# Optimization experiments

Hardware: AMD Instinct MI355X
Metric: run time of the kernel (lower is better)

The kernel has to match this reference:

```python
import jax, jax.numpy as jnp
import numpy as np
from jax import lax

B, S, D, L, HID = 256, 512, 64, 64, 256  # batch, seq_len, input_dim, latent_dim, MLP hidden


def setup_inputs() -> dict:
    key = jax.random.key(0)
    ks = jax.random.split(key, 16)
    sc = 0.05  # small init scale for MLP weights

    def eye_noise(k, n):
        # identity init (as in nn.Parameter(torch.eye)) plus small noise so inverse is non-trivial
        return jnp.eye(n, dtype=jnp.float32) + 0.05 * jax.random.normal(k, (n, n), dtype=jnp.float32)

    return {
        "x": jax.random.normal(ks[0], (B, S, D), dtype=jnp.float32),
        "eps": jax.random.normal(ks[1], (B, S, L), dtype=jnp.float32),
        "enc_w1": sc * jax.random.normal(ks[2], (D, HID), dtype=jnp.float32),
        "enc_b1": jnp.zeros((HID,), dtype=jnp.float32),
        "enc_w2": sc * jax.random.normal(ks[3], (HID, 2 * L), dtype=jnp.float32),
        "enc_b2": jnp.zeros((2 * L,), dtype=jnp.float32),
        "dec_w1": sc * jax.random.normal(ks[4], (L, HID), dtype=jnp.float32),
        "dec_b1": jnp.zeros((HID,), dtype=jnp.float32),
        "dec_w2": sc * jax.random.normal(ks[5], (HID, D), dtype=jnp.float32),
        "dec_b2": jnp.zeros((D,), dtype=jnp.float32),
        "A": eye_noise(ks[6], L),   # transition_matrix
        "Q": eye_noise(ks[7], L),   # process_covariance
        "Hm": eye_noise(ks[8], L),  # measurement_matrix
        "R": eye_noise(ks[9], L),   # measurement_covariance
    }


def reference(x, eps, enc_w1, enc_b1, enc_w2, enc_b2,
              dec_w1, dec_b1, dec_w2, dec_b2, A, Q, Hm, R):
    Bb, Ss, _ = x.shape
    # ---- encoder on all timesteps at once (no temporal dependency) ----
    h = jax.nn.relu(jnp.einsum('bsd,dh->bsh', x, enc_w1) + enc_b1)
    ml = jnp.einsum('bsh,hk->bsk', h, enc_w2) + enc_b2          # [B,S,2L]
    z_mean, z_logvar = jnp.split(ml, 2, axis=-1)                 # [B,S,L] each
    z = z_mean + eps * jnp.exp(0.5 * z_logvar)                   # reparameterize

    # ---- Kalman recursion; covariances don't depend on state in source, hoist ----
    AQ = A @ Q                                                   # z_pred_cov
    innov_cov = Hm @ AQ + R
    K = AQ @ jnp.linalg.inv(innov_cov)                           # kalman gain [L,L]

    def step(z_prev, inputs):
        x_t, z_t = inputs                                        # [B,D], [B,L]
        z_pred = z_prev @ A.T + z_t                              # (A @ z_prev^T)^T + z
        innovation = x_t - z_pred @ Hm.T
        z_up = z_pred + innovation @ K.T
        return z_up, z_up

    xs = (jnp.swapaxes(x, 0, 1), jnp.swapaxes(z, 0, 1))          # time-major [S,B,*]
    z0 = jnp.zeros((Bb, L), dtype=x.dtype)
    _, z_upd = lax.scan(step, z0, xs)                            # [S,B,L]
    z_upd = jnp.swapaxes(z_upd, 0, 1)                            # [B,S,L]

    # ---- decoder ----
    hd = jax.nn.relu(jnp.einsum('bsl,lh->bsh', z_upd, dec_w1) + dec_b1)
    x_recon = jax.nn.sigmoid(jnp.einsum('bsh,hd->bsd', hd, dec_w2) + dec_b2)

    return x_recon, z_mean.reshape(-1, L), z_logvar.reshape(-1, L)
```

## Files before the change

### kernel.cpp

```cpp
#include <hip/hip_runtime.h>
#include <hip/hip_bf16.h>


typedef short short8 __attribute__((ext_vector_type(8)));
typedef float f32x4 __attribute__((ext_vector_type(4)));

#define OUTSEG 8388608

__device__ __forceinline__ unsigned short f2bf(float f) {
    unsigned int u = __builtin_bit_cast(unsigned int, f);
    u += 0x7fffu + ((u >> 16) & 1u);
    return (unsigned short)(u >> 16);
}
__device__ __forceinline__ float bf2f(unsigned short h) {
    unsigned int u = ((unsigned int)h) << 16;
    return __builtin_bit_cast(float, u);
}
__device__ __forceinline__ float rlf(float v, int l) {
    return __builtin_bit_cast(float, __builtin_amdgcn_readlane(__builtin_bit_cast(int, v), l));
}
__device__ __forceinline__ float matvec_rl(const float* m, float z, float c) {
    float a0 = c, a1 = 0.f, a2 = 0.f, a3 = 0.f;
#pragma unroll
    for (int k = 0; k < 64; k += 4) {
        a0 = fmaf(m[k + 0], rlf(z, k + 0), a0);
        a1 = fmaf(m[k + 1], rlf(z, k + 1), a1);
        a2 = fmaf(m[k + 2], rlf(z, k + 2), a2);
        a3 = fmaf(m[k + 3], rlf(z, k + 3), a3);
    }
    return (a0 + a1) + (a2 + a3);
}
__device__ __forceinline__ void load_mrow(const float* Mp, int j, float* m) {
#pragma unroll
    for (int q = 0; q < 16; q++) {
        float4 v = *reinterpret_cast<const float4*>(&Mp[j * 64 + q * 4]);
        m[q * 4 + 0] = v.x; m[q * 4 + 1] = v.y;
        m[q * 4 + 2] = v.z; m[q * 4 + 3] = v.w;
    }
}

__device__ void mm64(const float* A, int lda, const float* B, int ldb,
                     float* C, int ldc, int mode, const float* Add, int ldadd,
                     int tid) {
    int i = tid & 63;
    int j0 = (tid >> 6) * 16;
    float acc[16];
#pragma unroll
    for (int jj = 0; jj < 16; jj++) acc[jj] = 0.f;
    for (int k = 0; k < 64; k++) {
        float a = A[i * lda + k];
#pragma unroll
        for (int jj = 0; jj < 16; jj++) acc[jj] += a * B[k * ldb + j0 + jj];
    }
#pragma unroll
    for (int jj = 0; jj < 16; jj++) {
        int j = j0 + jj;
        float v = acc[jj];
        if (mode == 1) v += Add[i * ldadd + j];
        if (mode == 2) v = ((i == j) ? 1.f : 0.f) - v;
        C[i * ldc + j] = v;
    }
}

__device__ void load64(const float* g, float* L, int tid) {
    for (int idx = tid; idx < 4096; idx += 256)
        L[(idx >> 6) * 65 + (idx & 63)] = g[idx];
}

__device__ void tr_tile(const float* src, int sld, unsigned short* dst, int dld,
                        int r0, int c0, int tid, float* LT) {
    int rr = tid >> 2, q = tid & 3;
#pragma unroll
    for (int u = 0; u < 4; u++) {
        float4 v = *reinterpret_cast<const float4*>(
            &src[(size_t)(r0 + rr) * sld + c0 + q * 16 + u * 4]);
        LT[rr * 65 + q * 16 + u * 4 + 0] = v.x;
        LT[rr * 65 + q * 16 + u * 4 + 1] = v.y;
        LT[rr * 65 + q * 16 + u * 4 + 2] = v.z;
        LT[rr * 65 + q * 16 + u * 4 + 3] = v.w;
    }
    __syncthreads();
    short8 s0, s1;
#pragma unroll
    for (int u = 0; u < 8; u++) s0[u] = (short)f2bf(LT[(q * 16 + u) * 65 + rr]);
#pragma unroll
    for (int u = 0; u < 8; u++) s1[u] = (short)f2bf(LT[(q * 16 + 8 + u) * 65 + rr]);
    *reinterpret_cast<short8*>(&dst[(size_t)(c0 + rr) * dld + r0 + q * 16]) = s0;
    *reinterpret_cast<short8*>(&dst[(size_t)(c0 + rr) * dld + r0 + q * 16 + 8]) = s1;
}

__global__ __launch_bounds__(256) void kprep(
    const float* __restrict__ Ain, const float* __restrict__ Qin,
    const float* __restrict__ Hin, const float* __restrict__ Rin,
    const float* __restrict__ ew1, const float* __restrict__ ew2,
    const float* __restrict__ dw1, const float* __restrict__ dw2,
    float* __restrict__ Mw, float* __restrict__ M16w,
    unsigned short* __restrict__ Gb, unsigned short* __restrict__ Kb,
    unsigned short* __restrict__ w1t, unsigned short* __restrict__ w2t,
    unsigned short* __restrict__ d1t, unsigned short* __restrict__ d2t) {
    __shared__ float La[64 * 65], Lb[64 * 65], Lc[64 * 65];
    __shared__ float aug[64 * 129];
    __shared__ int s_piv;
    __shared__ float s_pv;
    int tid = threadIdx.x;

    if (blockIdx.x != 0) {
        int t = blockIdx.x - 1;
        const float* src; unsigned short* dst; int sld, dld, r0, c0;
        if (t < 4)       { src = ew1; dst = w1t; sld = 256; dld = 64;  r0 = 0;             c0 = t * 64; }
        else if (t < 12) { int i = t - 4;  src = ew2; dst = w2t; sld = 128; dld = 256; r0 = (i >> 1) * 64; c0 = (i & 1) * 64; }
        else if (t < 16) { int i = t - 12; src = dw1; dst = d1t; sld = 256; dld = 64;  r0 = 0;             c0 = i * 64; }
        else             { int i = t - 16; src = dw2; dst = d2t; sld = 64;  dld = 256; r0 = i * 64;        c0 = 0; }
        tr_tile(src, sld, dst, dld, r0, c0, tid, La);
        return;
    }

    load64(Ain, La, tid);
    load64(Qin, Lb, tid);
    __syncthreads();
    mm64(La, 65, Lb, 65, Lc, 65, 0, nullptr, 0, tid);
    __syncthreads();
    load64(Hin, La, tid);
    load64(Rin, Lb, tid);
    __syncthreads();
    mm64(La, 65, Lc, 65, aug, 129, 1, Lb, 65, tid);
    for (int idx = tid; idx < 4096; idx += 256) {
        int i = idx >> 6, j = idx & 63;
        aug[i * 129 + 64 + j] = (i == j) ? 1.f : 0.f;
    }
    __syncthreads();

    for (int k = 0; k < 64; k++) {
        if (tid < 64) {
            float v = (tid >= k) ? fabsf(aug[tid * 129 + k]) : -1.f;
            int ix = tid;
#pragma unroll
            for (int off = 1; off < 64; off <<= 1) {
                float ov = __shfl_xor(v, off);
                int oi = __shfl_xor(ix, off);
                if (ov > v) { v = ov; ix = oi; }
            }
            if (tid == 0) { s_piv = ix; s_pv = aug[ix * 129 + k]; }
        }
        __syncthreads();
        int p = s_piv;
        float rp = 1.0f / s_pv;
        if (p != k) {
            for (int idx = tid; idx < 129; idx += 256) {
                float t1 = aug[k * 129 + idx];
                aug[k * 129 + idx] = aug[p * 129 + idx];
                aug[p * 129 + idx] = t1;
            }
            __syncthreads();
        }
        int i = tid & 63, jb = tid >> 6;
        float mlt = aug[i * 129 + k] * rp;
        float pv[33], rw[33];
#pragma unroll
        for (int jj = 0; jj < 33; jj++) {
            int j = jb + 4 * jj;
            if (j < 129) { pv[jj] = aug[k * 129 + j]; rw[jj] = aug[i * 129 + j]; }
        }
        __syncthreads();
#pragma unroll
        for (int jj = 0; jj < 33; jj++) {
            int j = jb + 4 * jj;
            if (j < 129) aug[i * 129 + j] = (i == k) ? pv[jj] * rp : rw[jj] - mlt * pv[jj];
        }
        __syncthreads();
    }

    mm64(Lc, 65, aug + 64, 129, Lb, 65, 0, nullptr, 0, tid);
    __syncthreads();
    mm64(Lb, 65, La, 65, Lc, 65, 2, nullptr, 0, tid);
    __syncthreads();
    for (int idx = tid; idx < 4096; idx += 256) {
        int i = idx >> 6, j = idx & 63;
        Kb[idx] = f2bf(Lb[i * 65 + j]);
        Gb[idx] = f2bf(Lc[i * 65 + j]);
    }
    load64(Ain, La, tid);
    __syncthreads();
    mm64(Lc, 65, La, 65, aug, 129, 0, nullptr, 0, tid);
    __syncthreads();
    for (int idx = tid; idx < 4096; idx += 256)
        Mw[idx] = aug[(idx >> 6) * 129 + (idx & 63)];
    __syncthreads();
    mm64(aug, 129, aug, 129, Lb, 65, 0, nullptr, 0, tid);
    __syncthreads();
    mm64(Lb, 65, Lb, 65, Lc, 65, 0, nullptr, 0, tid);
    __syncthreads();
    mm64(Lc, 65, Lc, 65, La, 65, 0, nullptr, 0, tid);
    __syncthreads();
    mm64(La, 65, La, 65, Lb, 65, 0, nullptr, 0, tid);
    __syncthreads();
    for (int idx = tid; idx < 4096; idx += 256)
        M16w[idx] = Lb[(idx >> 6) * 65 + (idx & 63)];
}

__global__ __launch_bounds__(256) void kenc(
    const float* __restrict__ x, const float* __restrict__ eps,
    const float* __restrict__ b1, const float* __restrict__ b2,
    const unsigned short* __restrict__ w1t, const unsigned short* __restrict__ w2t,
    const unsigned short* __restrict__ Gb, const unsigned short* __restrict__ Kb,
    const float* __restrict__ Mw, unsigned short* __restrict__ cbuf,
    float* __restrict__ Pbuf, float* __restrict__ zmean,
    float* __restrict__ zlogv) {
    __shared__ unsigned short Xs[64][72];
    __shared__ unsigned short Hs[64][264];
    __shared__ unsigned short Zs[64][72];
    int row0 = blockIdx.x * 64;
    int tid = threadIdx.x;
    int lane = tid & 63, w = tid >> 6;
    int ml = lane & 15, kg = lane >> 4;

    {
        int r = tid >> 2, c0 = (tid & 3) * 16;
        const float4* xp = reinterpret_cast<const float4*>(&x[(size_t)(row0 + r) * 64 + c0]);
        float4 v0 = xp[0], v1 = xp[1], v2 = xp[2], v3 = xp[3];
        short8 s0, s1;
        s0[0] = (short)f2bf(v0.x); s0[1] = (short)f2bf(v0.y);
        s0[2] = (short)f2bf(v0.z); s0[3] = (short)f2bf(v0.w);
        s0[4] = (short)f2bf(v1.x); s0[5] = (short)f2bf(v1.y);
        s0[6] = (short)f2bf(v1.z); s0[7] = (short)f2bf(v1.w);
        s1[0] = (short)f2bf(v2.x); s1[1] = (short)f2bf(v2.y);
        s1[2] = (short)f2bf(v2.z); s1[3] = (short)f2bf(v2.w);
        s1[4] = (short)f2bf(v3.x); s1[5] = (short)f2bf(v3.y);
        s1[6] = (short)f2bf(v3.z); s1[7] = (short)f2bf(v3.w);
        *reinterpret_cast<short8*>(&Xs[r][c0]) = s0;
        *reinterpret_cast<short8*>(&Xs[r][c0 + 8]) = s1;
    }
    __syncthreads();

    short8 afr[4][2];
#pragma unroll
    for (int mt = 0; mt < 4; mt++)
#pragma unroll
        for (int kb = 0; kb < 2; kb++)
            afr[mt][kb] = *reinterpret_cast<const short8*>(&Xs[mt * 16 + ml][kb * 32 + kg * 8]);

#pragma unroll
    for (int q = 0; q < 4; q++) {
        int nt = w * 4 + q;
        f32x4 acc[4];
#pragma unroll
        for (int mt = 0; mt < 4; mt++) acc[mt] = (f32x4){0.f, 0.f, 0.f, 0.f};
#pragma unroll
        for (int kb = 0; kb < 2; kb++) {
            short8 bfr = *reinterpret_cast<const short8*>(&w1t[(nt * 16 + ml) * 64 + kb * 32 + kg * 8]);
#pragma unroll
            for (int mt = 0; mt < 4; mt++)
                acc[mt] = __builtin_amdgcn_mfma_f32_16x16x32_bf16(afr[mt][kb], bfr, acc[mt], 0, 0, 0);
        }
        float bias = b1[nt * 16 + ml];
#pragma unroll
        for (int mt = 0; mt < 4; mt++)
#pragma unroll
            for (int i = 0; i < 4; i++) {
                float v = acc[mt][i] + bias;
                v = v > 0.f ? v : 0.f;
                Hs[mt * 16 + kg * 4 + i][nt * 16 + ml] = f2bf(v);
            }
    }
    __syncthreads();

    f32x4 acc2[2][4];
#pragma unroll
    for (int p = 0; p < 2; p++)
#pragma unroll
        for (int mt = 0; mt < 4; mt++) acc2[p][mt] = (f32x4){0.f, 0.f, 0.f, 0.f};
#pragma unroll
    for (int kb = 0; kb < 8; kb++) {
        short8 a2[4];
#pragma unroll
        for (int mt = 0; mt < 4; mt++)
            a2[mt] = *reinterpret_cast<const short8*>(&Hs[mt * 16 + ml][kb * 32 + kg * 8]);
#pragma unroll
        for (int p = 0; p < 2; p++) {
            int nt = w + 4 * p;
            short8 bfr = *reinterpret_cast<const short8*>(&w2t[(nt * 16 + ml) * 256 + kb * 32 + kg * 8]);
#pragma unroll
            for (int mt = 0; mt < 4; mt++)
                acc2[p][mt] = __builtin_amdgcn_mfma_f32_16x16x32_bf16(a2[mt], bfr, acc2[p][mt], 0, 0, 0);
        }
    }
    int colz = w * 16 + ml;
    float bm = b2[colz], bl = b2[64 + colz];
#pragma unroll
    for (int mt = 0; mt < 4; mt++)
#pragma unroll
        for (int i = 0; i < 4; i++) {
            int r = mt * 16 + kg * 4 + i;
            size_t grow = (size_t)(row0 + r);
            float zm = acc2[0][mt][i] + bm;
            float zl = acc2[1][mt][i] + bl;
            zmean[grow * 64 + colz] = zm;
            zlogv[grow * 64 + colz] = zl;
            float zz = zm + eps[grow * 64 + colz] * expf(0.5f * zl);
            Zs[r][colz] = f2bf(zz);
        }
    __syncthreads();

    f32x4 acc3[4];
#pragma unroll
    for (int mt = 0; mt < 4; mt++) acc3[mt] = (f32x4){0.f, 0.f, 0.f, 0.f};
    short8 az[4][2];
#pragma unroll
    for (int mt = 0; mt < 4; mt++)
#pragma unroll
        for (int kb = 0; kb < 2; kb++)
            az[mt][kb] = *reinterpret_cast<const short8*>(&Zs[mt * 16 + ml][kb * 32 + kg * 8]);
#pragma unroll
    for (int kb = 0; kb < 2; kb++) {
        short8 bg = *reinterpret_cast<const short8*>(&Gb[(w * 16 + ml) * 64 + kb * 32 + kg * 8]);
        short8 bk = *reinterpret_cast<const short8*>(&Kb[(w * 16 + ml) * 64 + kb * 32 + kg * 8]);
#pragma unroll
        for (int mt = 0; mt < 4; mt++)
            acc3[mt] = __builtin_amdgcn_mfma_f32_16x16x32_bf16(az[mt][kb], bg, acc3[mt], 0, 0, 0);
#pragma unroll
        for (int mt = 0; mt < 4; mt++)
            acc3[mt] = __builtin_amdgcn_mfma_f32_16x16x32_bf16(afr[mt][kb], bk, acc3[mt], 0, 0, 0);
    }
#pragma unroll
    for (int mt = 0; mt < 4; mt++)
#pragma unroll
        for (int i = 0; i < 4; i++)
            Xs[mt * 16 + kg * 4 + i][colz] = f2bf(acc3[mt][i]);
    __syncthreads();

    {
        int r = tid >> 2, c0 = (tid & 3) * 16;
        short8 s0 = *reinterpret_cast<const short8*>(&Xs[r][c0]);
        short8 s1 = *reinterpret_cast<const short8*>(&Xs[r][c0 + 8]);
        *reinterpret_cast<short8*>(&cbuf[(size_t)(row0 + r) * 64 + c0]) = s0;
        *reinterpret_cast<short8*>(&cbuf[(size_t)(row0 + r) * 64 + c0 + 8]) = s1;
    }

    {
        int j = lane;
        float m[64];
        load_mrow(Mw, j, m);
        unsigned short cv[16];
#pragma unroll
        for (int t = 0; t < 16; t++) cv[t] = Xs[w * 16 + t][j];
        float z = bf2f(cv[0]);
#pragma unroll
        for (int t = 1; t < 16; t++) z = matvec_rl(m, z, bf2f(cv[t]));
        int b = row0 >> 9;
        int chunk = ((row0 & 511) >> 4) + w;
        if (chunk != 31)
            Pbuf[((size_t)b * 32 + chunk + 1) * 64 + j] = z;
    }
}

__global__ __launch_bounds__(64) void kchain(const float* __restrict__ M16w,
                                             float* __restrict__ Pbuf) {
    int b = blockIdx.x, j = threadIdx.x;
    float m[64];
    load_mrow(M16w, j, m);
    float* P = Pbuf + (size_t)b * 32 * 64;
    P[j] = 0.f;
    float z = 0.f;
    for (int c = 1; c < 32; c++) {
        float f = P[c * 64 + j];
        z = matvec_rl(m, z, f);
        P[c * 64 + j] = z;
    }
}

__global__ __launch_bounds__(256) void kdec(float* __restrict__ xr,
                                            const float* __restrict__ db1,
                                            const float* __restrict__ db2,
                                            const unsigned short* __restrict__ d1t,
                                            const unsigned short* __restrict__ d2t,
                                            const float* __restrict__ Mw,
                                            const float* __restrict__ Pbuf,
                                            const unsigned short* __restrict__ cbuf) {
    __shared__ unsigned short Zs[64][72];
    __shared__ unsigned short Hs[64][264];
    int row0 = blockIdx.x * 64;
    int tid = threadIdx.x;
    int lane = tid & 63, w = tid >> 6;
    int ml = lane & 15, kg = lane >> 4;

    {
        int j = lane;
        int b = row0 >> 9;
        int chunk = ((row0 & 511) >> 4) + w;
        float m[64];
        load_mrow(Mw, j, m);
        float z = Pbuf[((size_t)b * 32 + chunk) * 64 + j];
        const unsigned short* cb = cbuf + ((size_t)row0 + w * 16) * 64;
        unsigned short cv[16];
#pragma unroll
        for (int t = 0; t < 16; t++) cv[t] = cb[t * 64 + j];
#pragma unroll
        for (int t = 0; t < 16; t++) {
            z = matvec_rl(m, z, bf2f(cv[t]));
            Zs[w * 16 + t][j] = f2bf(z);
        }
    }
    __syncthreads();

    short8 afr[4][2];
#pragma unroll
    for (int mt = 0; mt < 4; mt++)
#pragma unroll
        for (int kb = 0; kb < 2; kb++)
            afr[mt][kb] = *reinterpret_cast<const short8*>(&Zs[mt * 16 + ml][kb * 32 + kg * 8]);

#pragma unroll
    for (int q = 0; q < 4; q++) {
        int nt = w * 4 + q;
        f32x4 acc[4];
#pragma unroll
        for (int mt = 0; mt < 4; mt++) acc[mt] = (f32x4){0.f, 0.f, 0.f, 0.f};
#pragma unroll
        for (int kb = 0; kb < 2; kb++) {
            short8 bfr = *reinterpret_cast<const short8*>(&d1t[(nt * 16 + ml) * 64 + kb * 32 + kg * 8]);
#pragma unroll
            for (int mt = 0; mt < 4; mt++)
                acc[mt] = __builtin_amdgcn_mfma_f32_16x16x32_bf16(afr[mt][kb], bfr, acc[mt], 0, 0, 0);
        }
        float bias = db1[nt * 16 + ml];
#pragma unroll
        for (int mt = 0; mt < 4; mt++)
#pragma unroll
            for (int i = 0; i < 4; i++) {
                float v = acc[mt][i] + bias;
                v = v > 0.f ? v : 0.f;
                Hs[mt * 16 + kg * 4 + i][nt * 16 + ml] = f2bf(v);
            }
    }
    __syncthreads();

    f32x4 acc2[4];
#pragma unroll
    for (int mt = 0; mt < 4; mt++) acc2[mt] = (f32x4){0.f, 0.f, 0.f, 0.f};
#pragma unroll
    for (int kb = 0; kb < 8; kb++) {
        short8 bfr = *reinterpret_cast<const short8*>(&d2t[(w * 16 + ml) * 256 + kb * 32 + kg * 8]);
#pragma unroll
        for (int mt = 0; mt < 4; mt++) {
            short8 a2 = *reinterpret_cast<const short8*>(&Hs[mt * 16 + ml][kb * 32 + kg * 8]);
            acc2[mt] = __builtin_amdgcn_mfma_f32_16x16x32_bf16(a2, bfr, acc2[mt], 0, 0, 0);
        }
    }
    float bias2 = db2[w * 16 + ml];
#pragma unroll
    for (int mt = 0; mt < 4; mt++)
#pragma unroll
        for (int i = 0; i < 4; i++) {
            int r = mt * 16 + kg * 4 + i;
            float v = acc2[mt][i] + bias2;
            float s = 1.f / (1.f + expf(-v));
            xr[(size_t)(row0 + r) * 64 + w * 16 + ml] = s;
        }
}

extern "C" void kernel_launch(void* const* d_in, const int* in_sizes, int n_in,
                              void* d_out, int out_size, void* d_ws, size_t ws_size,
                              hipStream_t stream) {
    (void)in_sizes; (void)n_in; (void)out_size; (void)ws_size;
    const float* x      = (const float*)d_in[0];
    const float* eps    = (const float*)d_in[1];
    const float* enc_w1 = (const float*)d_in[2];
    const float* enc_b1 = (const float*)d_in[3];
    const float* enc_w2 = (const float*)d_in[4];
    const float* enc_b2 = (const float*)d_in[5];
    const float* dec_w1 = (const float*)d_in[6];
    const float* dec_b1 = (const float*)d_in[7];
    const float* dec_w2 = (const float*)d_in[8];
    const float* dec_b2 = (const float*)d_in[9];
    const float* Ain    = (const float*)d_in[10];
    const float* Qin    = (const float*)d_in[11];
    const float* Hin    = (const float*)d_in[12];
    const float* Rin    = (const float*)d_in[13];

    float* out   = (float*)d_out;
    float* xrec  = out;
    float* zmean = out + OUTSEG;
    float* zlogv = out + 2 * OUTSEG;

    char* ws = (char*)d_ws;
    float*          Mw   = (float*)(ws);
    float*          M16w = (float*)(ws + 16384);
    unsigned short* Gb   = (unsigned short*)(ws + 32768);
    unsigned short* Kb   = (unsigned short*)(ws + 40960);
    unsigned short* w1t  = (unsigned short*)(ws + 49152);
    unsigned short* w2t  = (unsigned short*)(ws + 81920);
    unsigned short* d1t  = (unsigned short*)(ws + 147456);
    unsigned short* d2t  = (unsigned short*)(ws + 180224);
    float*          Pbuf = (float*)(ws + 212992);
    unsigned short* cbuf = (unsigned short*)(ws + 2310144);

    hipLaunchKernelGGL(kprep, dim3(21), dim3(256), 0, stream,
                       Ain, Qin, Hin, Rin, enc_w1, enc_w2, dec_w1, dec_w2,
                       Mw, M16w, Gb, Kb, w1t, w2t, d1t, d2t);
    hipLaunchKernelGGL(kenc, dim3(2048), dim3(256), 0, stream,
                       x, eps, enc_b1, enc_b2, w1t, w2t, Gb, Kb, Mw, cbuf, Pbuf,
                       zmean, zlogv);
    hipLaunchKernelGGL(kchain, dim3(256), dim3(64), 0, stream, M16w, Pbuf);
    hipLaunchKernelGGL(kdec, dim3(2048), dim3(256), 0, stream,
                       xrec, dec_b1, dec_b2, d1t, d2t, Mw, Pbuf, cbuf);
}
```

Baseline: 424.2 us.

## Overlap Kalman matrix prep with encoder by splitting encoder into two kernels

The serial single-block Kalman precompute (gain, inverse, matrix powers) moves out of its own prep kernel into block 0 of a new encoder kernel, so it runs concurrently with the encoder MLP blocks. The encoder is split in two: kenc1 computes the MLP and stages bf16 z in the x_recon output buffer, and kenc2 applies G and K and does the intra-chunk recurrence. The Gauss-Jordan inverse is rewritten to keep rows in registers without pivoting, and kchain prefetches the next chunk value. The cost is an extra launch plus a global round trip for z, and dropping pivoting adds numerical risk.

```diff
diff --git a/kernel.cpp b/kernel.cpp
--- a/kernel.cpp
+++ b/kernel.cpp
@@ -37,34 +37,6 @@
         m[q * 4 + 0] = v.x; m[q * 4 + 1] = v.y;
         m[q * 4 + 2] = v.z; m[q * 4 + 3] = v.w;
     }
-}
-
-__device__ void mm64(const float* A, int lda, const float* B, int ldb,
-                     float* C, int ldc, int mode, const float* Add, int ldadd,
-                     int tid) {
-    int i = tid & 63;
-    int j0 = (tid >> 6) * 16;
-    float acc[16];
-#pragma unroll
-    for (int jj = 0; jj < 16; jj++) acc[jj] = 0.f;
-    for (int k = 0; k < 64; k++) {
-        float a = A[i * lda + k];
-#pragma unroll
-        for (int jj = 0; jj < 16; jj++) acc[jj] += a * B[k * ldb + j0 + jj];
-    }
-#pragma unroll
-    for (int jj = 0; jj < 16; jj++) {
-        int j = j0 + jj;
-        float v = acc[jj];
-        if (mode == 1) v += Add[i * ldadd + j];
-        if (mode == 2) v = ((i == j) ? 1.f : 0.f) - v;
-        C[i * ldc + j] = v;
-    }
-}
-
-__device__ void load64(const float* g, float* L, int tid) {
-    for (int idx = tid; idx < 4096; idx += 256)
-        L[(idx >> 6) * 65 + (idx & 63)] = g[idx];
 }
 
 __device__ void tr_tile(const float* src, int sld, unsigned short* dst, int dld,
@@ -89,128 +61,181 @@
     *reinterpret_cast<short8*>(&dst[(size_t)(c0 + rr) * dld + r0 + q * 16 + 8]) = s1;
 }
 
-__global__ __launch_bounds__(256) void kprep(
-    const float* __restrict__ Ain, const float* __restrict__ Qin,
-    const float* __restrict__ Hin, const float* __restrict__ Rin,
+__global__ __launch_bounds__(256) void ktr(
     const float* __restrict__ ew1, const float* __restrict__ ew2,
     const float* __restrict__ dw1, const float* __restrict__ dw2,
-    float* __restrict__ Mw, float* __restrict__ M16w,
-    unsigned short* __restrict__ Gb, unsigned short* __restrict__ Kb,
     unsigned short* __restrict__ w1t, unsigned short* __restrict__ w2t,
     unsigned short* __restrict__ d1t, unsigned short* __restrict__ d2t) {
-    __shared__ float La[64 * 65], Lb[64 * 65], Lc[64 * 65];
-    __shared__ float aug[64 * 129];
-    __shared__ int s_piv;
-    __shared__ float s_pv;
+    __shared__ float La[64 * 65];
     int tid = threadIdx.x;
-
-    if (blockIdx.x != 0) {
-        int t = blockIdx.x - 1;
-        const float* src; unsigned short* dst; int sld, dld, r0, c0;
-        if (t < 4)       { src = ew1; dst = w1t; sld = 256; dld = 64;  r0 = 0;             c0 = t * 64; }
-        else if (t < 12) { int i = t - 4;  src = ew2; dst = w2t; sld = 128; dld = 256; r0 = (i >> 1) * 64; c0 = (i & 1) * 64; }
-        else if (t < 16) { int i = t - 12; src = dw1; dst = d1t; sld = 256; dld = 64;  r0 = 0;             c0 = i * 64; }
-        else             { int i = t - 16; src = dw2; dst = d2t; sld = 64;  dld = 256; r0 = i * 64;        c0 = 0; }
-        tr_tile(src, sld, dst, dld, r0, c0, tid, La);
-        return;
-    }
-
-    load64(Ain, La, tid);
-    load64(Qin, Lb, tid);
-    __syncthreads();
-    mm64(La, 65, Lb, 65, Lc, 65, 0, nullptr, 0, tid);
-    __syncthreads();
-    load64(Hin, La, tid);
-    load64(Rin, Lb, tid);
-    __syncthreads();
-    mm64(La, 65, Lc, 65, aug, 129, 1, Lb, 65, tid);
+    int t = blockIdx.x;
+    const float* src; unsigned short* dst; int sld, dld, r0, c0;
+    if (t < 4)       { src = ew1; dst = w1t; sld = 256; dld = 64;  r0 = 0;             c0 = t * 64; }
+    else if (t < 12) { int i = t - 4;  src = ew2; dst = w2t; sld = 128; dld = 256; r0 = (i >> 1) * 64; c0 = (i & 1) * 64; }
+    else if (t < 16) { int i = t - 12; src = dw1; dst = d1t; sld = 256; dld = 64;  r0 = 0;             c0 = i * 64; }
+    else             { int i = t - 16; src = dw2; dst = d2t; sld = 64;  dld = 256; r0 = i * 64;        c0 = 0; }
+    tr_tile(src, sld, dst, dld, r0, c0, tid, La);
+}
+
+__device__ __noinline__ void mmc(const float* Ag, const float* Bg, float* Cg,
+                                 float* Lx, int mode, const float* Dg,
+                                 unsigned short* Cb, int tid) {
+    for (int idx = tid; idx < 4096; idx += 256)
+        Lx[(idx >> 6) * 68 + (idx & 63)] = Bg[idx];
+    __syncthreads();
+    int i = tid & 63, j0 = (tid >> 6) * 16;
+    float4 a4[16];
+#pragma unroll
+    for (int q = 0; q < 16; q++)
+        a4[q] = reinterpret_cast<const float4*>(Ag + i * 64)[q];
+    float acc[16];
+#pragma unroll
+    for (int jj = 0; jj < 16; jj++) acc[jj] = 0.f;
+#pragma unroll
+    for (int q = 0; q < 16; q++) {
+        float av[4] = {a4[q].x, a4[q].y, a4[q].z, a4[q].w};
+#pragma unroll
+        for (int t = 0; t < 4; t++) {
+            int k = q * 4 + t;
+            const float4* Br = reinterpret_cast<const float4*>(&Lx[k * 68 + j0]);
+            float4 b0 = Br[0], b1 = Br[1], b2 = Br[2], b3 = Br[3];
+            acc[0]  = fmaf(av[t], b0.x, acc[0]);
+            acc[1]  = fmaf(av[t], b0.y, acc[1]);
+            acc[2]  = fmaf(av[t], b0.z, acc[2]);
+            acc[3]  = fmaf(av[t], b0.w, acc[3]);
+            acc[4]  = fmaf(av[t], b1.x, acc[4]);
+            acc[5]  = fmaf(av[t], b1.y, acc[5]);
+            acc[6]  = fmaf(av[t], b1.z, acc[6]);
+            acc[7]  = fmaf(av[t], b1.w, acc[7]);
+            acc[8]  = fmaf(av[t], b2.x, acc[8]);
+            acc[9]  = fmaf(av[t], b2.y, acc[9]);
+            acc[10] = fmaf(av[t], b2.z, acc[10]);
+            acc[11] = fmaf(av[t], b2.w, acc[11]);
+            acc[12] = fmaf(av[t], b3.x, acc[12]);
+            acc[13] = fmaf(av[t], b3.y, acc[13]);
+            acc[14] = fmaf(av[t], b3.z, acc[14]);
+            acc[15] = fmaf(av[t], b3.w, acc[15]);
+        }
+    }
+#pragma unroll
+    for (int jj = 0; jj < 16; jj++) {
+        int j = j0 + jj;
+        float v = acc[jj];
+        if (mode == 1) v += Dg[i * 64 + j];
+        if (mode == 2) v = ((i == j) ? 1.f : 0.f) - v;
+        Cg[i * 64 + j] = v;
+        if (Cb) Cb[i * 64 + j] = f2bf(v);
+    }
+    __syncthreads();
+}
+
+__device__ void chain_block(char* smem, const float* Ain, const float* Qin,
+                            const float* Hin, const float* Rin,
+                            float* AQg, float* Sg, float* Kg, float* Gg,
+                            float* T1, float* T2, float* Mw, float* M16w,
+                            unsigned short* Gb, unsigned short* Kb) {
+    float* aug = (float*)smem;
+    float* Lx  = (float*)(smem + 33024);
+    float* prow2 = Lx;
+    float* mcol  = Lx + 128;
+    int tid = threadIdx.x;
+
+    mmc(Ain, Qin, AQg, Lx, 0, nullptr, nullptr, tid);
+    mmc(Hin, AQg, Sg, Lx, 1, Rin, nullptr, tid);
+
+    for (int idx = tid; idx < 8192; idx += 256) {
+        int i = idx & 63, j = idx >> 6;
+        float v = (j < 64) ? Sg[j * 64 + i] : AQg[(j - 64) * 64 + i];
+        aug[i * 129 + j] = v;
+    }
+    __syncthreads();
+
+    int i = tid & 63, jb = tid >> 6;
+    float r[32];
+#pragma unroll
+    for (int u = 0; u < 32; u++) r[u] = aug[i * 129 + jb + 4 * u];
+    __syncthreads();
+
+    for (int k = 0; k < 64; k++) {
+        if (i == k) {
+#pragma unroll
+            for (int q = 0; q < 8; q++) {
+                float4 v4 = {r[4 * q], r[4 * q + 1], r[4 * q + 2], r[4 * q + 3]};
+                *reinterpret_cast<float4*>(&prow2[jb * 32 + 4 * q]) = v4;
+            }
+        }
+        if (jb == (k & 3)) {
+            int usel = k >> 2;
+            float v = r[0];
+#pragma unroll
+            for (int u = 1; u < 32; u++) v = (u == usel) ? r[u] : v;
+            mcol[i] = v;
+        }
+        __syncthreads();
+        float pv = prow2[(k & 3) * 32 + (k >> 2)];
+        float rp = 1.0f / pv;
+        float m = (i == k) ? (1.0f - rp) : mcol[i] * rp;
+#pragma unroll
+        for (int q = 0; q < 8; q++) {
+            float4 p4 = *reinterpret_cast<const float4*>(&prow2[jb * 32 + 4 * q]);
+            r[4 * q + 0] = fmaf(-m, p4.x, r[4 * q + 0]);
+            r[4 * q + 1] = fmaf(-m, p4.y, r[4 * q + 1]);
+            r[4 * q + 2] = fmaf(-m, p4.z, r[4 * q + 2]);
+            r[4 * q + 3] = fmaf(-m, p4.w, r[4 * q + 3]);
+        }
+        __syncthreads();
+    }
+
+    float* Ktmp = aug;
+#pragma unroll
+    for (int u = 16; u < 32; u++) {
+        int jc = jb + 4 * (u - 16);
+        Ktmp[jc * 64 + i] = r[u];
+    }
+    __syncthreads();
     for (int idx = tid; idx < 4096; idx += 256) {
-        int i = idx >> 6, j = idx & 63;
-        aug[i * 129 + 64 + j] = (i == j) ? 1.f : 0.f;
-    }
-    __syncthreads();
-
-    for (int k = 0; k < 64; k++) {
-        if (tid < 64) {
-            float v = (tid >= k) ? fabsf(aug[tid * 129 + k]) : -1.f;
-            int ix = tid;
-#pragma unroll
-            for (int off = 1; off < 64; off <<= 1) {
-                float ov = __shfl_xor(v, off);
-                int oi = __shfl_xor(ix, off);
-                if (ov > v) { v = ov; ix = oi; }
-            }
-            if (tid == 0) { s_piv = ix; s_pv = aug[ix * 129 + k]; }
-        }
-        __syncthreads();
-        int p = s_piv;
-        float rp = 1.0f / s_pv;
-        if (p != k) {
-            for (int idx = tid; idx < 129; idx += 256) {
-                float t1 = aug[k * 129 + idx];
-                aug[k * 129 + idx] = aug[p * 129 + idx];
-                aug[p * 129 + idx] = t1;
-            }
-            __syncthreads();
-        }
-        int i = tid & 63, jb = tid >> 6;
-        float mlt = aug[i * 129 + k] * rp;
-        float pv[33], rw[33];
-#pragma unroll
-        for (int jj = 0; jj < 33; jj++) {
-            int j = jb + 4 * jj;
-            if (j < 129) { pv[jj] = aug[k * 129 + j]; rw[jj] = aug[i * 129 + j]; }
-        }
-        __syncthreads();
-#pragma unroll
-        for (int jj = 0; jj < 33; jj++) {
-            int j = jb + 4 * jj;
-            if (j < 129) aug[i * 129 + j] = (i == k) ? pv[jj] * rp : rw[jj] - mlt * pv[jj];
-        }
-        __syncthreads();
-    }
-
-    mm64(Lc, 65, aug + 64, 129, Lb, 65, 0, nullptr, 0, tid);
-    __syncthreads();
-    mm64(Lb, 65, La, 65, Lc, 65, 2, nullptr, 0, tid);
-    __syncthreads();
-    for (int idx = tid; idx < 4096; idx += 256) {
-        int i = idx >> 6, j = idx & 63;
-        Kb[idx] = f2bf(Lb[i * 65 + j]);
-        Gb[idx] = f2bf(Lc[i * 65 + j]);
-    }
-    load64(Ain, La, tid);
-    __syncthreads();
-    mm64(Lc, 65, La, 65, aug, 129, 0, nullptr, 0, tid);
-    __syncthreads();
-    for (int idx = tid; idx < 4096; idx += 256)
-        Mw[idx] = aug[(idx >> 6) * 129 + (idx & 63)];
-    __syncthreads();
-    mm64(aug, 129, aug, 129, Lb, 65, 0, nullptr, 0, tid);
-    __syncthreads();
-    mm64(Lb, 65, Lb, 65, Lc, 65, 0, nullptr, 0, tid);
-    __syncthreads();
-    mm64(Lc, 65, Lc, 65, La, 65, 0, nullptr, 0, tid);
-    __syncthreads();
-    mm64(La, 65, La, 65, Lb, 65, 0, nullptr, 0, tid);
-    __syncthreads();
-    for (int idx = tid; idx < 4096; idx += 256)
-        M16w[idx] = Lb[(idx >> 6) * 65 + (idx & 63)];
-}
-
-__global__ __launch_bounds__(256) void kenc(
+        float v = Ktmp[idx];
+        Kg[idx] = v;
+        Kb[idx] = f2bf(v);
+    }
+    __syncthreads();
+
+    mmc(Kg, Hin, Gg, Lx, 2, nullptr, Gb, tid);
+    mmc(Gg, Ain, Mw, Lx, 0, nullptr, nullptr, tid);
+    mmc(Mw, Mw, T1, Lx, 0, nullptr, nullptr, tid);
+    mmc(T1, T1, T2, Lx, 0, nullptr, nullptr, tid);
+    mmc(T2, T2, T1, Lx, 0, nullptr, nullptr, tid);
+    mmc(T1, T1, M16w, Lx, 0, nullptr, nullptr, tid);
+}
+
+__global__ __launch_bounds__(256) void kenc1(
     const float* __restrict__ x, const float* __restrict__ eps,
     const float* __restrict__ b1, const float* __restrict__ b2,
     const unsigned short* __restrict__ w1t, const unsigned short* __restrict__ w2t,
-    const unsigned short* __restrict__ Gb, const unsigned short* __restrict__ Kb,
-    const float* __restrict__ Mw, unsigned short* __restrict__ cbuf,
-    float* __restrict__ Pbuf, float* __restrict__ zmean,
-    float* __restrict__ zlogv) {
-    __shared__ unsigned short Xs[64][72];
-    __shared__ unsigned short Hs[64][264];
-    __shared__ unsigned short Zs[64][72];
-    int row0 = blockIdx.x * 64;
+    unsigned short* __restrict__ zstg, float* __restrict__ zmean,
+    float* __restrict__ zlogv,
+    const float* __restrict__ Ain, const float* __restrict__ Qin,
+    const float* __restrict__ Hin, const float* __restrict__ Rin,
+    float* __restrict__ AQg, float* __restrict__ Sg, float* __restrict__ Kg,
+    float* __restrict__ Gg, float* __restrict__ T1, float* __restrict__ T2,
+    float* __restrict__ Mw, float* __restrict__ M16w,
+    unsigned short* __restrict__ Gb, unsigned short* __restrict__ Kb) {
+    __shared__ __align__(16) char smem[52224];
     int tid = threadIdx.x;
+
+    if (blockIdx.x == 0) {
+        chain_block(smem, Ain, Qin, Hin, Rin, AQg, Sg, Kg, Gg, T1, T2,
+                    Mw, M16w, Gb, Kb);
+        return;
+    }
+
+    typedef unsigned short (*T72)[72];
+    typedef unsigned short (*T264)[264];
+    T72  Xs = (T72)(smem);
+    T264 Hs = (T264)(smem + 9216);
+    T72  Zs = (T72)(smem + 43008);
+
+    int row0 = (blockIdx.x - 1) * 64;
     int lane = tid & 63, w = tid >> 6;
     int ml = lane & 15, kg = lane >> 4;
 
@@ -301,37 +326,73 @@
         }
     __syncthreads();
 
+    {
+        int r = tid >> 2, c0 = (tid & 3) * 16;
+        short8 s0 = *reinterpret_cast<const short8*>(&Zs[r][c0]);
+        short8 s1 = *reinterpret_cast<const short8*>(&Zs[r][c0 + 8]);
+        *reinterpret_cast<short8*>(&zstg[(size_t)(row0 + r) * 64 + c0]) = s0;
+        *reinterpret_cast<short8*>(&zstg[(size_t)(row0 + r) * 64 + c0 + 8]) = s1;
+    }
+}
+
+__global__ __launch_bounds__(256) void kenc2(
+    const float* __restrict__ x, const unsigned short* __restrict__ zstg,
+    const unsigned short* __restrict__ Gb, const unsigned short* __restrict__ Kb,
+    const float* __restrict__ Mw, unsigned short* __restrict__ cbuf,
+    float* __restrict__ Pbuf) {
+    __shared__ unsigned short Xs[64][72];
+    __shared__ unsigned short Cs[64][72];
+    int row0 = blockIdx.x * 64;
+    int tid = threadIdx.x;
+    int lane = tid & 63, w = tid >> 6;
+    int ml = lane & 15, kg = lane >> 4;
+
+    {
+        int r = tid >> 2, c0 = (tid & 3) * 16;
+        const float4* xp = reinterpret_cast<const float4*>(&x[(size_t)(row0 + r) * 64 + c0]);
+        float4 v0 = xp[0], v1 = xp[1], v2 = xp[2], v3 = xp[3];
+        short8 s0, s1;
+        s0[0] = (short)f2bf(v0.x); s0[1] = (short)f2bf(v0.y);
+        s0[2] = (short)f2bf(v0.z); s0[3] = (short)f2bf(v0.w);
+        s0[4] = (short)f2bf(v1.x); s0[5] = (short)f2bf(v1.y);
+        s0[6] = (short)f2bf(v1.z); s0[7] = (short)f2bf(v1.w);
+        s1[0] = (short)f2bf(v2.x); s1[1] = (short)f2bf(v2.y);
+        s1[2] = (short)f2bf(v2.z); s1[3] = (short)f2bf(v2.w);
+        s1[4] = (short)f2bf(v3.x); s1[5] = (short)f2bf(v3.y);
+        s1[6] = (short)f2bf(v3.z); s1[7] = (short)f2bf(v3.w);
+        *reinterpret_cast<short8*>(&Xs[r][c0]) = s0;
+        *reinterpret_cast<short8*>(&Xs[r][c0 + 8]) = s1;
+    }
+    __syncthreads();
+
+    int colz = w * 16 + ml;
     f32x4 acc3[4];
 #pragma unroll
     for (int mt = 0; mt < 4; mt++) acc3[mt] = (f32x4){0.f, 0.f, 0.f, 0.f};
-    short8 az[4][2];
-#pragma unroll
-    for (int mt = 0; mt < 4; mt++)
-#pragma unroll
-        for (int kb = 0; kb < 2; kb++)
-            az[mt][kb] = *reinterpret_cast<const short8*>(&Zs[mt * 16 + ml][kb * 32 + kg * 8]);
 #pragma unroll
     for (int kb = 0; kb < 2; kb++) {
         short8 bg = *reinterpret_cast<const short8*>(&Gb[(w * 16 + ml) * 64 + kb * 32 + kg * 8]);
         short8 bk = *reinterpret_cast<const short8*>(&Kb[(w * 16 + ml) * 64 + kb * 32 + kg * 8]);
 #pragma unroll
-        for (int mt = 0; mt < 4; mt++)
-            acc3[mt] = __builtin_amdgcn_mfma_f32_16x16x32_bf16(az[mt][kb], bg, acc3[mt], 0, 0, 0);
-#pragma unroll
-        for (int mt = 0; mt < 4; mt++)
-            acc3[mt] = __builtin_amdgcn_mfma_f32_16x16x32_bf16(afr[mt][kb], bk, acc3[mt], 0, 0, 0);
+        for (int mt = 0; mt < 4; mt++) {
+            short8 az = *reinterpret_cast<const short8*>(
+                &zstg[(size_t)(row0 + mt * 16 + ml) * 64 + kb * 32 + kg * 8]);
+            acc3[mt] = __builtin_amdgcn_mfma_f32_16x16x32_bf16(az, bg, acc3[mt], 0, 0, 0);
+            short8 ax = *reinterpret_cast<const short8*>(&Xs[mt * 16 + ml][kb * 32 + kg * 8]);
+            acc3[mt] = __builtin_amdgcn_mfma_f32_16x16x32_bf16(ax, bk, acc3[mt], 0, 0, 0);
+        }
     }
 #pragma unroll
     for (int mt = 0; mt < 4; mt++)
 #pragma unroll
         for (int i = 0; i < 4; i++)
-            Xs[mt * 16 + kg * 4 + i][colz] = f2bf(acc3[mt][i]);
+            Cs[mt * 16 + kg * 4 + i][colz] = f2bf(acc3[mt][i]);
     __syncthreads();
 
     {
         int r = tid >> 2, c0 = (tid & 3) * 16;
-        short8 s0 = *reinterpret_cast<const short8*>(&Xs[r][c0]);
-        short8 s1 = *reinterpret_cast<const short8*>(&Xs[r][c0 + 8]);
+        short8 s0 = *reinterpret_cast<const short8*>(&Cs[r][c0]);
+        short8 s1 = *reinterpret_cast<const short8*>(&Cs[r][c0 + 8]);
         *reinterpret_cast<short8*>(&cbuf[(size_t)(row0 + r) * 64 + c0]) = s0;
         *reinterpret_cast<short8*>(&cbuf[(size_t)(row0 + r) * 64 + c0 + 8]) = s1;
     }
@@ -342,7 +403,7 @@
         load_mrow(Mw, j, m);
         unsigned short cv[16];
 #pragma unroll
-        for (int t = 0; t < 16; t++) cv[t] = Xs[w * 16 + t][j];
+        for (int t = 0; t < 16; t++) cv[t] = Cs[w * 16 + t][j];
         float z = bf2f(cv[0]);
 #pragma unroll
         for (int t = 1; t < 16; t++) z = matvec_rl(m, z, bf2f(cv[t]));
@@ -359,10 +420,12 @@
     float m[64];
     load_mrow(M16w, j, m);
     float* P = Pbuf + (size_t)b * 32 * 64;
+    float fnext = P[64 + j];
     P[j] = 0.f;
     float z = 0.f;
     for (int c = 1; c < 32; c++) {
-        float f = P[c * 64 + j];
+        float f = fnext;
+        if (c < 31) fnext = P[(c + 1) * 64 + j];
         z = matvec_rl(m, z, f);
         P[c * 64 + j] = z;
     }
@@ -481,25 +544,34 @@
     float* xrec  = out;
     float* zmean = out + OUTSEG;
     float* zlogv = out + 2 * OUTSEG;
+    unsigned short* zstg = (unsigned short*)xrec;
 
     char* ws = (char*)d_ws;
     float*          Mw   = (float*)(ws);
     float*          M16w = (float*)(ws + 16384);
-    unsigned short* Gb   = (unsigned short*)(ws + 32768);
-    unsigned short* Kb   = (unsigned short*)(ws + 40960);
-    unsigned short* w1t  = (unsigned short*)(ws + 49152);
-    unsigned short* w2t  = (unsigned short*)(ws + 81920);
-    unsigned short* d1t  = (unsigned short*)(ws + 147456);
-    unsigned short* d2t  = (unsigned short*)(ws + 180224);
-    float*          Pbuf = (float*)(ws + 212992);
-    unsigned short* cbuf = (unsigned short*)(ws + 2310144);
-
-    hipLaunchKernelGGL(kprep, dim3(21), dim3(256), 0, stream,
-                       Ain, Qin, Hin, Rin, enc_w1, enc_w2, dec_w1, dec_w2,
-                       Mw, M16w, Gb, Kb, w1t, w2t, d1t, d2t);
-    hipLaunchKernelGGL(kenc, dim3(2048), dim3(256), 0, stream,
-                       x, eps, enc_b1, enc_b2, w1t, w2t, Gb, Kb, Mw, cbuf, Pbuf,
-                       zmean, zlogv);
+    float*          AQg  = (float*)(ws + 32768);
+    float*          Sg   = (float*)(ws + 49152);
+    float*          Kg   = (float*)(ws + 65536);
+    float*          Gg   = (float*)(ws + 81920);
+    float*          T1   = (float*)(ws + 98304);
+    float*          T2   = (float*)(ws + 114688);
+    unsigned short* Gb   = (unsigned short*)(ws + 131072);
+    unsigned short* Kb   = (unsigned short*)(ws + 139264);
+    unsigned short* w1t  = (unsigned short*)(ws + 147456);
+    unsigned short* w2t  = (unsigned short*)(ws + 180224);
+    unsigned short* d1t  = (unsigned short*)(ws + 245760);
+    unsigned short* d2t  = (unsigned short*)(ws + 278528);
+    float*          Pbuf = (float*)(ws + 311296);
+    unsigned short* cbuf = (unsigned short*)(ws + 2408448);
+
+    hipLaunchKernelGGL(ktr, dim3(20), dim3(256), 0, stream,
+                       enc_w1, enc_w2, dec_w1, dec_w2, w1t, w2t, d1t, d2t);
+    hipLaunchKernelGGL(kenc1, dim3(2049), dim3(256), 0, stream,
+                       x, eps, enc_b1, enc_b2, w1t, w2t, zstg, zmean, zlogv,
+                       Ain, Qin, Hin, Rin, AQg, Sg, Kg, Gg, T1, T2, Mw, M16w,
+                       Gb, Kb);
+    hipLaunchKernelGGL(kenc2, dim3(2048), dim3(256), 0, stream,
+                       x, zstg, Gb, Kb, Mw, cbuf, Pbuf);
     hipLaunchKernelGGL(kchain, dim3(256), dim3(64), 0, stream, M16w, Pbuf);
     hipLaunchKernelGGL(kdec, dim3(2048), dim3(256), 0, stream,
                        xrec, dec_b1, dec_b2, d1t, d2t, Mw, Pbuf, cbuf);
```

Result: slower. 926.1 us (+118.3%).
